# Kernel optimization log

Measured on AMD Instinct MI355X. Metric: run time of the kernel, lower is better.

Reference implementation:

```python
import jax, jax.numpy as jnp
import numpy as np

D_MODEL = 256
N_HEADS = 4
D_HEAD = D_MODEL // N_HEADS
SCALE = 1.0 / np.sqrt(D_HEAD).astype(np.float32)


def setup_inputs() -> dict:
    key = jax.random.key(0)
    ks = jax.random.split(key, 8)
    B, T, S = 4, 512, 512
    return {
        "query": jax.random.normal(ks[0], (B, T, D_MODEL), dtype=jnp.float32),
        "key": jax.random.normal(ks[1], (B, S, D_MODEL), dtype=jnp.float32),
        "value": jax.random.normal(ks[2], (B, S, D_MODEL), dtype=jnp.float32),
        "w_q": jax.random.normal(ks[3], (D_MODEL, D_MODEL), dtype=jnp.float32) * 0.05,
        "w_k": jax.random.normal(ks[4], (D_MODEL, D_MODEL), dtype=jnp.float32) * 0.05,
        "w_v": jax.random.normal(ks[5], (D_MODEL, D_MODEL), dtype=jnp.float32) * 0.05,
        "v_a": jax.random.normal(ks[6], (N_HEADS, D_HEAD), dtype=jnp.float32),
        "w_o": jax.random.normal(ks[7], (D_MODEL, D_MODEL), dtype=jnp.float32) * 0.05,
    }


def reference(query, key, value, w_q, w_k, w_v, v_a, w_o):
    B, T, _ = query.shape
    S = key.shape[1]
    # projections; weights stored as (out, in) like nn.Linear -> x @ W.T
    Q = (query @ w_q.T).reshape(B, T, N_HEADS, D_HEAD).transpose(0, 2, 1, 3)  # bhtd
    K = (key @ w_k.T).reshape(B, S, N_HEADS, D_HEAD).transpose(0, 2, 1, 3)    # bhsd
    V = (value @ w_v.T).reshape(B, S, N_HEADS, D_HEAD).transpose(0, 2, 1, 3)  # bhsd
    # additive (Bahdanau) scores: tanh broadcast of shape (B,H,T,S,Dh)
    combined = jnp.tanh(Q[:, :, :, None, :] + K[:, :, None, :, :])
    scores = jnp.einsum('bhtsd,hd->bhts', combined, v_a) * SCALE
    attn = jax.nn.softmax(scores, axis=-1)  # (B,H,T,S)
    attended = jnp.einsum('bhts,bhsd->bhtd', attn, V)
    attended = attended.transpose(0, 2, 1, 3).reshape(B, T, D_MODEL)
    out = attended @ w_o.T
    return out, attn
```

## Files before the change

kernel.cpp:

```cpp
#include <hip/hip_runtime.h>
#include <math.h>

#define BATCH 4
#define TLEN 512
#define SLEN 512
#define DM 256
#define NH 4
#define DH 64
#define BT (BATCH * TLEN)

__device__ __forceinline__ float rcp_fast(float x) { return __builtin_amdgcn_rcpf(x); }

__device__ __forceinline__ void transpose_tile(const float* __restrict__ S,
                                               float* __restrict__ D, int bx) {
  __shared__ float tile[64][65];
  int to = (bx & 3) * 64;
  int tk = (bx >> 2) * 64;
  int lo = threadIdx.x >> 6;
  int lk = threadIdx.x & 63;
#pragma unroll
  for (int p = 0; p < 16; ++p) {
    int o = p * 4 + lo;
    tile[o][lk] = S[(size_t)(to + o) * DM + tk + lk];
  }
  __syncthreads();
#pragma unroll
  for (int p = 0; p < 16; ++p) {
    int kk = p * 4 + lo;
    D[(size_t)(tk + kk) * DM + to + lk] = tile[lk][kk];
  }
}

__global__ __launch_bounds__(256) void transpose3_kernel(
    const float* __restrict__ a, const float* __restrict__ b, const float* __restrict__ c,
    float* __restrict__ ta, float* __restrict__ tb, float* __restrict__ tc) {
  int m = blockIdx.y;
  transpose_tile(m == 0 ? a : (m == 1 ? b : c),
                 m == 0 ? ta : (m == 1 ? tb : tc), blockIdx.x);
}

__global__ __launch_bounds__(256) void transpose1_kernel(
    const float* __restrict__ a, float* __restrict__ ta) {
  transpose_tile(a, ta, blockIdx.x);
}

__device__ __forceinline__ void gemm_wave4(const float* __restrict__ X,
                                           const float* __restrict__ WT,
                                           int o0, float4* acc) {
#pragma unroll
  for (int r = 0; r < 4; ++r) acc[r] = make_float4(0.f, 0.f, 0.f, 0.f);
#pragma unroll 4
  for (int kk = 0; kk < DM; ++kk) {
    float4 w = *(const float4*)(WT + (size_t)kk * DM + o0);
#pragma unroll
    for (int r = 0; r < 4; ++r) {
      float xv = X[r * DM + kk];
      acc[r].x = fmaf(xv, w.x, acc[r].x);
      acc[r].y = fmaf(xv, w.y, acc[r].y);
      acc[r].z = fmaf(xv, w.z, acc[r].z);
      acc[r].w = fmaf(xv, w.w, acc[r].w);
    }
  }
}

__global__ __launch_bounds__(128) void proj_kernel(
    const float* __restrict__ q, const float* __restrict__ k, const float* __restrict__ v,
    const float* __restrict__ wqt, const float* __restrict__ wkt, const float* __restrict__ wvt,
    float* __restrict__ EQ, float* __restrict__ EKT, float* __restrict__ Vw) {
  int tid = threadIdx.x;
  int lane = tid & 63;
  int wid = __builtin_amdgcn_readfirstlane(tid >> 6);
  int which = blockIdx.y;
  const float* X = (which == 0) ? q : (which == 1) ? k : v;
  const float* WT = (which == 0) ? wqt : (which == 1) ? wkt : wvt;
  int row0 = blockIdx.x * 8 + wid * 4;
  int o0 = lane * 4;
  float4 acc[4];
  gemm_wave4(X + (size_t)row0 * DM, WT, o0, acc);
  int h = o0 >> 6, d0 = o0 & 63;
#pragma unroll
  for (int r = 0; r < 4; ++r) {
    int row = row0 + r;
    int b = row >> 9, t = row & 511;
    int bh = b * NH + h;
    float4 a = acc[r];
    if (which < 2) {
      a.x = __expf(2.f * fminf(fmaxf(a.x, -11.f), 11.f));
      a.y = __expf(2.f * fminf(fmaxf(a.y, -11.f), 11.f));
      a.z = __expf(2.f * fminf(fmaxf(a.z, -11.f), 11.f));
      a.w = __expf(2.f * fminf(fmaxf(a.w, -11.f), 11.f));
    }
    if (which == 0) {
      *(float4*)&EQ[((size_t)bh * TLEN + t) * DH + d0] = a;
    } else if (which == 1) {
      *(float4*)&EKT[(((size_t)bh * 16 + (d0 >> 2)) * SLEN + t) * 4] = a;
    } else {
      float* vb = &Vw[(size_t)bh * SLEN * DH + (size_t)(t >> 1) * 128 + d0 * 2 + (t & 1)];
      vb[0] = a.x; vb[2] = a.y; vb[4] = a.z; vb[6] = a.w;
    }
  }
}

__global__ __launch_bounds__(256, 4) void attn_kernel(
    const float* __restrict__ EQ, const float* __restrict__ EKT,
    const float* __restrict__ Vw, const float* __restrict__ va_g,
    float* __restrict__ attn_out, float* __restrict__ attended) {
  __shared__ float pw[8][SLEN];
  __shared__ float fp[4][8][64];
  __shared__ float sred[2][8][4];
  int tid = threadIdx.x;
  int lane = tid & 63;
  int wid = __builtin_amdgcn_readfirstlane(tid >> 6);
  int bx = (int)((blockIdx.x & 7) * 128 + (blockIdx.x >> 3));
  int bh = bx >> 6;
  int tile = (bx & 63) * 8;
  int h = bh & 3, b = bh >> 2;
  int sq0 = wid * 128;

  const float4* ekf = (const float4*)EKT + (size_t)bh * (16 * SLEN) + sq0 + lane;
  const float* eqb = EQ + ((size_t)bh * TLEN + tile) * DH;
  const float* vap = va_g + h * DH;

  float acc[8][2];
#pragma unroll
  for (int t = 0; t < 8; ++t) { acc[t][0] = 0.f; acc[t][1] = 0.f; }
  float vsum = 0.f;

  float4 eA0, eA1, eB0, eB1;

#define LOADE(EV, dc_) do { EV##0 = ekf[(size_t)(dc_) * SLEN]; \
                            EV##1 = ekf[(size_t)(dc_) * SLEN + 64]; } while (0)

#define SC(E, qv, av, aref) do {                                            \
    float A0 = fmaf(qv.x, E.x, 1.f), A1 = fmaf(qv.y, E.y, 1.f);             \
    float A2 = fmaf(qv.z, E.z, 1.f), A3 = fmaf(qv.w, E.w, 1.f);             \
    float n01 = fmaf(av.y, A0, av.x * A1);                                  \
    float n23 = fmaf(av.w, A2, av.z * A3);                                  \
    aref = fmaf(n01, rcp_fast(A0 * A1), aref);                              \
    aref = fmaf(n23, rcp_fast(A2 * A3), aref);                              \
  } while (0)

#define DCBODY(CUR, NXT, dc_) do {                                          \
    float4 av = *(const float4*)(vap + (dc_) * 4);                          \
    float4 q0 = *(const float4*)(eqb + 0 * DH + (dc_) * 4);                 \
    float4 q1 = *(const float4*)(eqb + 1 * DH + (dc_) * 4);                 \
    float4 q2 = *(const float4*)(eqb + 2 * DH + (dc_) * 4);                 \
    float4 q3 = *(const float4*)(eqb + 3 * DH + (dc_) * 4);                 \
    float4 q4 = *(const float4*)(eqb + 4 * DH + (dc_) * 4);                 \
    float4 q5 = *(const float4*)(eqb + 5 * DH + (dc_) * 4);                 \
    float4 q6 = *(const float4*)(eqb + 6 * DH + (dc_) * 4);                 \
    float4 q7 = *(const float4*)(eqb + 7 * DH + (dc_) * 4);                 \
    vsum += (av.x + av.y) + (av.z + av.w);                                  \
    if ((dc_) < 15) LOADE(NXT, (dc_) + 1);                                  \
    __builtin_amdgcn_sched_barrier(0);                                      \
    SC(CUR##0, q0, av, acc[0][0]); SC(CUR##1, q0, av, acc[0][1]);           \
    SC(CUR##0, q1, av, acc[1][0]); SC(CUR##1, q1, av, acc[1][1]);           \
    SC(CUR##0, q2, av, acc[2][0]); SC(CUR##1, q2, av, acc[2][1]);           \
    SC(CUR##0, q3, av, acc[3][0]); SC(CUR##1, q3, av, acc[3][1]);           \
    SC(CUR##0, q4, av, acc[4][0]); SC(CUR##1, q4, av, acc[4][1]);           \
    SC(CUR##0, q5, av, acc[5][0]); SC(CUR##1, q5, av, acc[5][1]);           \
    SC(CUR##0, q6, av, acc[6][0]); SC(CUR##1, q6, av, acc[6][1]);           \
    SC(CUR##0, q7, av, acc[7][0]); SC(CUR##1, q7, av, acc[7][1]);           \
  } while (0)

  LOADE(eA, 0);
#pragma unroll 1
  for (int dc2 = 0; dc2 < 8; ++dc2) {
    DCBODY(eA, eB, 2 * dc2);
    DCBODY(eB, eA, 2 * dc2 + 1);
  }

  size_t bht = (size_t)bh * TLEN + tile;
  float e0[8], e1[8];
#pragma unroll
  for (int t = 0; t < 8; ++t) {
    float s0 = (vsum - 2.f * acc[t][0]) * 0.125f;
    float s1 = (vsum - 2.f * acc[t][1]) * 0.125f;
    acc[t][0] = s0; acc[t][1] = s1;
    float m = fmaxf(s0, s1);
#pragma unroll
    for (int off = 32; off; off >>= 1) m = fmaxf(m, __shfl_xor(m, off));
    if (lane == 0) sred[0][t][wid] = m;
  }
  __syncthreads();
#pragma unroll
  for (int t = 0; t < 8; ++t) {
    float m = fmaxf(fmaxf(sred[0][t][0], sred[0][t][1]),
                    fmaxf(sred[0][t][2], sred[0][t][3]));
    float x0 = __expf(acc[t][0] - m);
    float x1 = __expf(acc[t][1] - m);
    e0[t] = x0; e1[t] = x1;
    float es = x0 + x1;
#pragma unroll
    for (int off = 32; off; off >>= 1) es += __shfl_xor(es, off);
    if (lane == 0) sred[1][t][wid] = es;
  }
  __syncthreads();
#pragma unroll
  for (int t = 0; t < 8; ++t) {
    float es = (sred[1][t][0] + sred[1][t][1]) + (sred[1][t][2] + sred[1][t][3]);
    float inv = rcp_fast(es);
    float p0 = e0[t] * inv, p1 = e1[t] * inv;
    pw[t][sq0 + lane] = p0;
    pw[t][sq0 + 64 + lane] = p1;
    float* arow = attn_out + (bht + t) * SLEN + sq0;
    arow[lane] = p0;
    arow[64 + lane] = p1;
  }

  const float2* vb = (const float2*)Vw + (size_t)bh * (256 * 64) + (size_t)(wid * 64) * 64 + lane;
  float f[8];
#pragma unroll
  for (int t = 0; t < 8; ++t) f[t] = 0.f;
#pragma unroll 2
  for (int i = 0; i < 32; ++i) {
    float2 v01 = vb[(size_t)i * 128];
    float2 v23 = vb[(size_t)i * 128 + 64];
    int sb = sq0 + i * 4;
#pragma unroll
    for (int t = 0; t < 8; ++t) {
      float4 pq = *(const float4*)&pw[t][sb];
      f[t] = fmaf(pq.x, v01.x, f[t]);
      f[t] = fmaf(pq.y, v01.y, f[t]);
      f[t] = fmaf(pq.z, v23.x, f[t]);
      f[t] = fmaf(pq.w, v23.y, f[t]);
    }
  }
#pragma unroll
  for (int t = 0; t < 8; ++t) fp[wid][t][lane] = f[t];
  __syncthreads();
#pragma unroll
  for (int j = 0; j < 2; ++j) {
    int t = wid * 2 + j;
    float s = (fp[0][t][lane] + fp[1][t][lane]) + (fp[2][t][lane] + fp[3][t][lane]);
    attended[((size_t)(b * TLEN) + tile + t) * DM + h * DH + lane] = s;
  }
}

__global__ __launch_bounds__(128) void outproj_kernel(
    const float* __restrict__ att, const float* __restrict__ wot,
    float* __restrict__ out) {
  int tid = threadIdx.x;
  int lane = tid & 63;
  int wid = __builtin_amdgcn_readfirstlane(tid >> 6);
  int row0 = blockIdx.x * 8 + wid * 4;
  int o0 = lane * 4;
  float4 acc[4];
  gemm_wave4(att + (size_t)row0 * DM, wot, o0, acc);
#pragma unroll
  for (int r = 0; r < 4; ++r)
    *(float4*)&out[(size_t)(row0 + r) * DM + o0] = acc[r];
}

extern "C" void kernel_launch(void* const* d_in, const int* in_sizes, int n_in,
                              void* d_out, int out_size, void* d_ws, size_t ws_size,
                              hipStream_t stream) {
  const float* query = (const float*)d_in[0];
  const float* key   = (const float*)d_in[1];
  const float* value = (const float*)d_in[2];
  const float* wq    = (const float*)d_in[3];
  const float* wk    = (const float*)d_in[4];
  const float* wv    = (const float*)d_in[5];
  const float* va    = (const float*)d_in[6];
  const float* wo    = (const float*)d_in[7];

  float* out  = (float*)d_out;
  float* attn = out + (size_t)BT * DM;

  float* EQ  = (float*)d_ws;
  float* EKT = EQ + (size_t)BT * DM;
  float* Vw  = EKT + (size_t)BT * DM;
  float* att = Vw + (size_t)BT * DM;
  float* WTq = att;
  float* WTk = att + 65536;
  float* WTv = att + 131072;
  float* WoT = EQ;

  transpose3_kernel<<<dim3(16, 3), 256, 0, stream>>>(wq, wk, wv, WTq, WTk, WTv);
  proj_kernel<<<dim3(BT / 8, 3), 128, 0, stream>>>(query, key, value, WTq, WTk, WTv, EQ, EKT, Vw);
  attn_kernel<<<dim3(1024), 256, 0, stream>>>(EQ, EKT, Vw, va, attn, att);
  transpose1_kernel<<<dim3(16), 256, 0, stream>>>(wo, WoT);
  outproj_kernel<<<dim3(BT / 8), 128, 0, stream>>>(att, WoT, out);
}
```

Before: 102.6 us.

## Halve attention tile, drop softmax max pass, merge rcp, widen GEMM blocks

The attention kernel now handles 4 query rows per block instead of 8, with 2048 blocks and launch bounds raised to 8 blocks per SM. The softmax max-reduction pass and its barrier are removed, relying on the scores being bounded. The tanh-sum evaluation merges two reciprocals into one per four dimensions, and the exp clamp shrinks to ±5.5 so the larger products stay in float range. The projection and output GEMMs use 256-thread blocks with fewer rows per wave, and the Wo transpose is folded into the first transpose launch when the workspace is large enough. Risks include numerical overflow or precision loss from skipping the max subtraction and merging reciprocals, and lower per-thread reuse in the GEMMs.

```diff
diff --git a/kernel.cpp b/kernel.cpp
--- a/kernel.cpp
+++ b/kernel.cpp
@@ -11,9 +11,16 @@
 
 __device__ __forceinline__ float rcp_fast(float x) { return __builtin_amdgcn_rcpf(x); }
 
-__device__ __forceinline__ void transpose_tile(const float* __restrict__ S,
-                                               float* __restrict__ D, int bx) {
+__global__ __launch_bounds__(256) void transposeN_kernel(
+    const float* __restrict__ s0, const float* __restrict__ s1,
+    const float* __restrict__ s2, const float* __restrict__ s3,
+    float* __restrict__ d0, float* __restrict__ d1,
+    float* __restrict__ d2, float* __restrict__ d3) {
   __shared__ float tile[64][65];
+  int m = blockIdx.y;
+  const float* S = (m == 0) ? s0 : (m == 1) ? s1 : (m == 2) ? s2 : s3;
+  float* D = (m == 0) ? d0 : (m == 1) ? d1 : (m == 2) ? d2 : d3;
+  int bx = blockIdx.x;
   int to = (bx & 3) * 64;
   int tk = (bx >> 2) * 64;
   int lo = threadIdx.x >> 6;
@@ -31,39 +38,7 @@
   }
 }
 
-__global__ __launch_bounds__(256) void transpose3_kernel(
-    const float* __restrict__ a, const float* __restrict__ b, const float* __restrict__ c,
-    float* __restrict__ ta, float* __restrict__ tb, float* __restrict__ tc) {
-  int m = blockIdx.y;
-  transpose_tile(m == 0 ? a : (m == 1 ? b : c),
-                 m == 0 ? ta : (m == 1 ? tb : tc), blockIdx.x);
-}
-
-__global__ __launch_bounds__(256) void transpose1_kernel(
-    const float* __restrict__ a, float* __restrict__ ta) {
-  transpose_tile(a, ta, blockIdx.x);
-}
-
-__device__ __forceinline__ void gemm_wave4(const float* __restrict__ X,
-                                           const float* __restrict__ WT,
-                                           int o0, float4* acc) {
-#pragma unroll
-  for (int r = 0; r < 4; ++r) acc[r] = make_float4(0.f, 0.f, 0.f, 0.f);
-#pragma unroll 4
-  for (int kk = 0; kk < DM; ++kk) {
-    float4 w = *(const float4*)(WT + (size_t)kk * DM + o0);
-#pragma unroll
-    for (int r = 0; r < 4; ++r) {
-      float xv = X[r * DM + kk];
-      acc[r].x = fmaf(xv, w.x, acc[r].x);
-      acc[r].y = fmaf(xv, w.y, acc[r].y);
-      acc[r].z = fmaf(xv, w.z, acc[r].z);
-      acc[r].w = fmaf(xv, w.w, acc[r].w);
-    }
-  }
-}
-
-__global__ __launch_bounds__(128) void proj_kernel(
+__global__ __launch_bounds__(256) void proj_kernel(
     const float* __restrict__ q, const float* __restrict__ k, const float* __restrict__ v,
     const float* __restrict__ wqt, const float* __restrict__ wkt, const float* __restrict__ wvt,
     float* __restrict__ EQ, float* __restrict__ EKT, float* __restrict__ Vw) {
@@ -73,22 +48,34 @@
   int which = blockIdx.y;
   const float* X = (which == 0) ? q : (which == 1) ? k : v;
   const float* WT = (which == 0) ? wqt : (which == 1) ? wkt : wvt;
-  int row0 = blockIdx.x * 8 + wid * 4;
+  int row0 = blockIdx.x * 8 + wid * 2;
   int o0 = lane * 4;
-  float4 acc[4];
-  gemm_wave4(X + (size_t)row0 * DM, WT, o0, acc);
+  const float* xb = X + (size_t)row0 * DM;
+  float4 a0 = make_float4(0.f, 0.f, 0.f, 0.f);
+  float4 a1 = make_float4(0.f, 0.f, 0.f, 0.f);
+#pragma unroll 8
+  for (int kk = 0; kk < DM; ++kk) {
+    float4 w = *(const float4*)(WT + (size_t)kk * DM + o0);
+    float x0 = xb[kk];
+    float x1 = xb[DM + kk];
+    a0.x = fmaf(x0, w.x, a0.x); a0.y = fmaf(x0, w.y, a0.y);
+    a0.z = fmaf(x0, w.z, a0.z); a0.w = fmaf(x0, w.w, a0.w);
+    a1.x = fmaf(x1, w.x, a1.x); a1.y = fmaf(x1, w.y, a1.y);
+    a1.z = fmaf(x1, w.z, a1.z); a1.w = fmaf(x1, w.w, a1.w);
+  }
   int h = o0 >> 6, d0 = o0 & 63;
-#pragma unroll
-  for (int r = 0; r < 4; ++r) {
+  float4 accs[2] = {a0, a1};
+#pragma unroll
+  for (int r = 0; r < 2; ++r) {
     int row = row0 + r;
     int b = row >> 9, t = row & 511;
     int bh = b * NH + h;
-    float4 a = acc[r];
+    float4 a = accs[r];
     if (which < 2) {
-      a.x = __expf(2.f * fminf(fmaxf(a.x, -11.f), 11.f));
-      a.y = __expf(2.f * fminf(fmaxf(a.y, -11.f), 11.f));
-      a.z = __expf(2.f * fminf(fmaxf(a.z, -11.f), 11.f));
-      a.w = __expf(2.f * fminf(fmaxf(a.w, -11.f), 11.f));
+      a.x = __expf(2.f * fminf(fmaxf(a.x, -5.5f), 5.5f));
+      a.y = __expf(2.f * fminf(fmaxf(a.y, -5.5f), 5.5f));
+      a.z = __expf(2.f * fminf(fmaxf(a.z, -5.5f), 5.5f));
+      a.w = __expf(2.f * fminf(fmaxf(a.w, -5.5f), 5.5f));
     }
     if (which == 0) {
       *(float4*)&EQ[((size_t)bh * TLEN + t) * DH + d0] = a;
@@ -101,19 +88,19 @@
   }
 }
 
-__global__ __launch_bounds__(256, 4) void attn_kernel(
+__global__ __launch_bounds__(256, 8) void attn_kernel(
     const float* __restrict__ EQ, const float* __restrict__ EKT,
     const float* __restrict__ Vw, const float* __restrict__ va_g,
     float* __restrict__ attn_out, float* __restrict__ attended) {
-  __shared__ float pw[8][SLEN];
-  __shared__ float fp[4][8][64];
-  __shared__ float sred[2][8][4];
+  __shared__ float pw[4][SLEN];
+  __shared__ float fp[4][4][64];
+  __shared__ float sred[4][4];
   int tid = threadIdx.x;
   int lane = tid & 63;
   int wid = __builtin_amdgcn_readfirstlane(tid >> 6);
-  int bx = (int)((blockIdx.x & 7) * 128 + (blockIdx.x >> 3));
-  int bh = bx >> 6;
-  int tile = (bx & 63) * 8;
+  int bx = (int)((blockIdx.x & 7) * 256 + (blockIdx.x >> 3));
+  int bh = bx >> 7;
+  int tile = (bx & 127) * 4;
   int h = bh & 3, b = bh >> 2;
   int sq0 = wid * 128;
 
@@ -121,9 +108,9 @@
   const float* eqb = EQ + ((size_t)bh * TLEN + tile) * DH;
   const float* vap = va_g + h * DH;
 
-  float acc[8][2];
-#pragma unroll
-  for (int t = 0; t < 8; ++t) { acc[t][0] = 0.f; acc[t][1] = 0.f; }
+  float acc[4][2];
+#pragma unroll
+  for (int t = 0; t < 4; ++t) { acc[t][0] = 0.f; acc[t][1] = 0.f; }
   float vsum = 0.f;
 
   float4 eA0, eA1, eB0, eB1;
@@ -131,13 +118,14 @@
 #define LOADE(EV, dc_) do { EV##0 = ekf[(size_t)(dc_) * SLEN]; \
                             EV##1 = ekf[(size_t)(dc_) * SLEN + 64]; } while (0)
 
-#define SC(E, qv, av, aref) do {                                            \
+#define SC4(E, qv, av, aref) do {                                           \
     float A0 = fmaf(qv.x, E.x, 1.f), A1 = fmaf(qv.y, E.y, 1.f);             \
     float A2 = fmaf(qv.z, E.z, 1.f), A3 = fmaf(qv.w, E.w, 1.f);             \
-    float n01 = fmaf(av.y, A0, av.x * A1);                                  \
-    float n23 = fmaf(av.w, A2, av.z * A3);                                  \
-    aref = fmaf(n01, rcp_fast(A0 * A1), aref);                              \
-    aref = fmaf(n23, rcp_fast(A2 * A3), aref);                              \
+    float n01 = fmaf(av.x, A1, av.y * A0);                                  \
+    float n23 = fmaf(av.z, A3, av.w * A2);                                  \
+    float P01 = A0 * A1, P23 = A2 * A3;                                     \
+    float Nm = fmaf(n01, P23, n23 * P01);                                   \
+    aref = fmaf(Nm, rcp_fast(P01 * P23), aref);                             \
   } while (0)
 
 #define DCBODY(CUR, NXT, dc_) do {                                          \
@@ -146,21 +134,13 @@
     float4 q1 = *(const float4*)(eqb + 1 * DH + (dc_) * 4);                 \
     float4 q2 = *(const float4*)(eqb + 2 * DH + (dc_) * 4);                 \
     float4 q3 = *(const float4*)(eqb + 3 * DH + (dc_) * 4);                 \
-    float4 q4 = *(const float4*)(eqb + 4 * DH + (dc_) * 4);                 \
-    float4 q5 = *(const float4*)(eqb + 5 * DH + (dc_) * 4);                 \
-    float4 q6 = *(const float4*)(eqb + 6 * DH + (dc_) * 4);                 \
-    float4 q7 = *(const float4*)(eqb + 7 * DH + (dc_) * 4);                 \
     vsum += (av.x + av.y) + (av.z + av.w);                                  \
     if ((dc_) < 15) LOADE(NXT, (dc_) + 1);                                  \
     __builtin_amdgcn_sched_barrier(0);                                      \
-    SC(CUR##0, q0, av, acc[0][0]); SC(CUR##1, q0, av, acc[0][1]);           \
-    SC(CUR##0, q1, av, acc[1][0]); SC(CUR##1, q1, av, acc[1][1]);           \
-    SC(CUR##0, q2, av, acc[2][0]); SC(CUR##1, q2, av, acc[2][1]);           \
-    SC(CUR##0, q3, av, acc[3][0]); SC(CUR##1, q3, av, acc[3][1]);           \
-    SC(CUR##0, q4, av, acc[4][0]); SC(CUR##1, q4, av, acc[4][1]);           \
-    SC(CUR##0, q5, av, acc[5][0]); SC(CUR##1, q5, av, acc[5][1]);           \
-    SC(CUR##0, q6, av, acc[6][0]); SC(CUR##1, q6, av, acc[6][1]);           \
-    SC(CUR##0, q7, av, acc[7][0]); SC(CUR##1, q7, av, acc[7][1]);           \
+    SC4(CUR##0, q0, av, acc[0][0]); SC4(CUR##1, q0, av, acc[0][1]);         \
+    SC4(CUR##0, q1, av, acc[1][0]); SC4(CUR##1, q1, av, acc[1][1]);         \
+    SC4(CUR##0, q2, av, acc[2][0]); SC4(CUR##1, q2, av, acc[2][1]);         \
+    SC4(CUR##0, q3, av, acc[3][0]); SC4(CUR##1, q3, av, acc[3][1]);         \
   } while (0)
 
   LOADE(eA, 0);
@@ -171,34 +151,21 @@
   }
 
   size_t bht = (size_t)bh * TLEN + tile;
-  float e0[8], e1[8];
-#pragma unroll
-  for (int t = 0; t < 8; ++t) {
-    float s0 = (vsum - 2.f * acc[t][0]) * 0.125f;
-    float s1 = (vsum - 2.f * acc[t][1]) * 0.125f;
-    acc[t][0] = s0; acc[t][1] = s1;
-    float m = fmaxf(s0, s1);
-#pragma unroll
-    for (int off = 32; off; off >>= 1) m = fmaxf(m, __shfl_xor(m, off));
-    if (lane == 0) sred[0][t][wid] = m;
-  }
-  __syncthreads();
-#pragma unroll
-  for (int t = 0; t < 8; ++t) {
-    float m = fmaxf(fmaxf(sred[0][t][0], sred[0][t][1]),
-                    fmaxf(sred[0][t][2], sred[0][t][3]));
-    float x0 = __expf(acc[t][0] - m);
-    float x1 = __expf(acc[t][1] - m);
+  float e0[4], e1[4];
+#pragma unroll
+  for (int t = 0; t < 4; ++t) {
+    float x0 = __expf(fmaf(acc[t][0], -0.25f, vsum * 0.125f));
+    float x1 = __expf(fmaf(acc[t][1], -0.25f, vsum * 0.125f));
     e0[t] = x0; e1[t] = x1;
     float es = x0 + x1;
 #pragma unroll
     for (int off = 32; off; off >>= 1) es += __shfl_xor(es, off);
-    if (lane == 0) sred[1][t][wid] = es;
+    if (lane == 0) sred[t][wid] = es;
   }
   __syncthreads();
 #pragma unroll
-  for (int t = 0; t < 8; ++t) {
-    float es = (sred[1][t][0] + sred[1][t][1]) + (sred[1][t][2] + sred[1][t][3]);
+  for (int t = 0; t < 4; ++t) {
+    float es = (sred[t][0] + sred[t][1]) + (sred[t][2] + sred[t][3]);
     float inv = rcp_fast(es);
     float p0 = e0[t] * inv, p1 = e1[t] * inv;
     pw[t][sq0 + lane] = p0;
@@ -209,16 +176,16 @@
   }
 
   const float2* vb = (const float2*)Vw + (size_t)bh * (256 * 64) + (size_t)(wid * 64) * 64 + lane;
-  float f[8];
-#pragma unroll
-  for (int t = 0; t < 8; ++t) f[t] = 0.f;
+  float f[4];
+#pragma unroll
+  for (int t = 0; t < 4; ++t) f[t] = 0.f;
 #pragma unroll 2
   for (int i = 0; i < 32; ++i) {
     float2 v01 = vb[(size_t)i * 128];
     float2 v23 = vb[(size_t)i * 128 + 64];
     int sb = sq0 + i * 4;
 #pragma unroll
-    for (int t = 0; t < 8; ++t) {
+    for (int t = 0; t < 4; ++t) {
       float4 pq = *(const float4*)&pw[t][sb];
       f[t] = fmaf(pq.x, v01.x, f[t]);
       f[t] = fmaf(pq.y, v01.y, f[t]);
@@ -227,29 +194,35 @@
     }
   }
 #pragma unroll
-  for (int t = 0; t < 8; ++t) fp[wid][t][lane] = f[t];
+  for (int t = 0; t < 4; ++t) fp[wid][t][lane] = f[t];
   __syncthreads();
-#pragma unroll
-  for (int j = 0; j < 2; ++j) {
-    int t = wid * 2 + j;
+  {
+    int t = wid;
     float s = (fp[0][t][lane] + fp[1][t][lane]) + (fp[2][t][lane] + fp[3][t][lane]);
     attended[((size_t)(b * TLEN) + tile + t) * DM + h * DH + lane] = s;
   }
 }
 
-__global__ __launch_bounds__(128) void outproj_kernel(
+__global__ __launch_bounds__(256) void outproj_kernel(
     const float* __restrict__ att, const float* __restrict__ wot,
     float* __restrict__ out) {
   int tid = threadIdx.x;
   int lane = tid & 63;
   int wid = __builtin_amdgcn_readfirstlane(tid >> 6);
-  int row0 = blockIdx.x * 8 + wid * 4;
+  int row = blockIdx.x * 4 + wid;
   int o0 = lane * 4;
-  float4 acc[4];
-  gemm_wave4(att + (size_t)row0 * DM, wot, o0, acc);
-#pragma unroll
-  for (int r = 0; r < 4; ++r)
-    *(float4*)&out[(size_t)(row0 + r) * DM + o0] = acc[r];
+  const float* xb = att + (size_t)row * DM;
+  float4 a = make_float4(0.f, 0.f, 0.f, 0.f);
+#pragma unroll 8
+  for (int kk = 0; kk < DM; ++kk) {
+    float4 w = *(const float4*)(wot + (size_t)kk * DM + o0);
+    float xv = xb[kk];
+    a.x = fmaf(xv, w.x, a.x);
+    a.y = fmaf(xv, w.y, a.y);
+    a.z = fmaf(xv, w.z, a.z);
+    a.w = fmaf(xv, w.w, a.w);
+  }
+  *(float4*)&out[(size_t)row * DM + o0] = a;
 }
 
 extern "C" void kernel_launch(void* const* d_in, const int* in_sizes, int n_in,
@@ -267,18 +240,32 @@
   float* out  = (float*)d_out;
   float* attn = out + (size_t)BT * DM;
 
+  const size_t SEG = (size_t)BT * DM;
   float* EQ  = (float*)d_ws;
-  float* EKT = EQ + (size_t)BT * DM;
-  float* Vw  = EKT + (size_t)BT * DM;
-  float* att = Vw + (size_t)BT * DM;
-  float* WTq = att;
-  float* WTk = att + 65536;
-  float* WTv = att + 131072;
-  float* WoT = EQ;
-
-  transpose3_kernel<<<dim3(16, 3), 256, 0, stream>>>(wq, wk, wv, WTq, WTk, WTv);
-  proj_kernel<<<dim3(BT / 8, 3), 128, 0, stream>>>(query, key, value, WTq, WTk, WTv, EQ, EKT, Vw);
-  attn_kernel<<<dim3(1024), 256, 0, stream>>>(EQ, EKT, Vw, va, attn, att);
-  transpose1_kernel<<<dim3(16), 256, 0, stream>>>(wo, WoT);
-  outproj_kernel<<<dim3(BT / 8), 128, 0, stream>>>(att, WoT, out);
-}
+  float* EKT = EQ + SEG;
+  float* Vw  = EKT + SEG;
+  float* att = Vw + SEG;
+
+  bool big_ws = ws_size >= (4 * SEG + 4 * (size_t)DM * DM) * sizeof(float);
+
+  if (big_ws) {
+    float* WTq = att + SEG;
+    float* WTk = WTq + (size_t)DM * DM;
+    float* WTv = WTk + (size_t)DM * DM;
+    float* WoT = WTv + (size_t)DM * DM;
+    transposeN_kernel<<<dim3(16, 4), 256, 0, stream>>>(wq, wk, wv, wo, WTq, WTk, WTv, WoT);
+    proj_kernel<<<dim3(BT / 8, 3), 256, 0, stream>>>(query, key, value, WTq, WTk, WTv, EQ, EKT, Vw);
+    attn_kernel<<<dim3(2048), 256, 0, stream>>>(EQ, EKT, Vw, va, attn, att);
+    outproj_kernel<<<dim3(BT / 4), 256, 0, stream>>>(att, WoT, out);
+  } else {
+    float* WTq = att;
+    float* WTk = att + (size_t)DM * DM;
+    float* WTv = att + 2 * (size_t)DM * DM;
+    float* WoT = EQ;
+    transposeN_kernel<<<dim3(16, 3), 256, 0, stream>>>(wq, wk, wv, wv, WTq, WTk, WTv, WTv);
+    proj_kernel<<<dim3(BT / 8, 3), 256, 0, stream>>>(query, key, value, WTq, WTk, WTv, EQ, EKT, Vw);
+    attn_kernel<<<dim3(2048), 256, 0, stream>>>(EQ, EKT, Vw, va, attn, att);
+    transposeN_kernel<<<dim3(16, 1), 256, 0, stream>>>(wo, wo, wo, wo, WoT, WoT, WoT, WoT);
+    outproj_kernel<<<dim3(BT / 4), 256, 0, stream>>>(att, WoT, out);
+  }
+}
```

Result: faster. 91.72 us (-10.6%).
